# Performance work log

Hardware: AMD Instinct MI355X
Metric: run time of the kernel (lower is better)

The kernel has to match this reference:

```python
import jax, jax.numpy as jnp
import numpy as np

B, L = 4, 2048
D_Q = D_K = D_V = 512
D_MODEL = 512
H = 8  # heads; head dim = D_MODEL // H = 64


def _conv1x1(x, W, b):
    # Conv1d with kernel_size=1 == pointwise linear over channels.
    # x: (B, C_in, L), W: (C_out, C_in), b: (C_out,) -> (B, C_out, L)
    return jnp.einsum('oc,bcl->bol', W, x) + b[None, :, None]


def setup_inputs() -> dict:
    key = jax.random.key(0)
    ks = jax.random.split(key, 12)
    s = 0.02
    return {
        'q': jax.random.normal(ks[0], (B, D_Q, L), jnp.float32),
        'k': jax.random.normal(ks[1], (B, D_K, L), jnp.float32),
        'v': jax.random.normal(ks[2], (B, D_V, L), jnp.float32),
        'input_mask': jnp.ones((B, 1, L), jnp.float32),
        'Wq': jax.random.normal(ks[3], (D_MODEL, D_Q), jnp.float32) * s,
        'bq': jax.random.normal(ks[4], (D_MODEL,), jnp.float32) * s,
        'Wk': jax.random.normal(ks[5], (D_MODEL, D_K), jnp.float32) * s,
        'bk': jax.random.normal(ks[6], (D_MODEL,), jnp.float32) * s,
        'Wv': jax.random.normal(ks[7], (D_MODEL, D_V), jnp.float32) * s,
        'bv': jax.random.normal(ks[8], (D_MODEL,), jnp.float32) * s,
        'Wout': jax.random.normal(ks[9], (D_V, D_MODEL), jnp.float32) * s,
        'bout': jax.random.normal(ks[10], (D_V,), jnp.float32) * s,
    }


def reference(q, k, v, input_mask, Wq, bq, Wk, bk, Wv, bv, Wout, bout):
    Bq, _, Lq = q.shape
    qh = _conv1x1(q, Wq, bq).reshape(Bq, H, -1, Lq)  # (B,H,D,L)
    kh = _conv1x1(k, Wk, bk).reshape(Bq, H, -1, Lq)
    vh = _conv1x1(v, Wv, bv).reshape(Bq, H, -1, Lq)
    Dh = qh.shape[2]
    scale = 1.0 / jnp.sqrt(jnp.asarray(Dh, qh.dtype))
    scores = jnp.einsum('bhdl,bhdn->bhln', qh, kh) * scale  # (B,H,L,L)
    # total_mask = ~input_mask[:, 0:1, :].bool(); True -> masked keys
    pad = input_mask[:, 0:1, :] <= 0.5  # (B,1,L_k)
    scores = jnp.where(pad[:, None, :, :], jnp.asarray(-1e9, scores.dtype), scores)
    attn = jax.nn.softmax(scores, axis=-1)  # attn_dropout is None in module
    out = jnp.einsum('bhdn,bhln->bhdl', vh, attn).reshape(Bq, -1, Lq)  # (B,d_model,L)
    # self.dropout is identity at inference; final 1x1 conv projection
    return _conv1x1(out, Wout, bout)  # (B, d_v, L)
```

## Files before the change

### kernel.cpp

```cpp
#include <hip/hip_runtime.h>
#include <hip/hip_bf16.h>


#define BB  4
#define LL  2048
#define CC  512
#define HH  8
#define DHH 64

typedef __attribute__((ext_vector_type(8)))  short bf16x8;
typedef __attribute__((ext_vector_type(4)))  short bf16x4;
typedef __attribute__((ext_vector_type(16))) float f32x16;
typedef __attribute__((ext_vector_type(2)))  unsigned uint2v;
typedef __attribute__((ext_vector_type(4)))  unsigned uint4v;

using us = unsigned short;

#if __has_builtin(__builtin_amdgcn_exp2f)
#define EXP2(x) __builtin_amdgcn_exp2f(x)
#else
#define EXP2(x) __expf(0.6931471805599453f * (x))
#endif

__device__ __forceinline__ int swz(int r) { return (r + (r >> 3)) & 7; }

__device__ __forceinline__ us f2bu(float x) {
    unsigned u = __float_as_uint(x);
    return (us)((u + 0x7FFFu + ((u >> 16) & 1u)) >> 16);
}
__device__ __forceinline__ unsigned pk2(float a, float b) {
    unsigned r;
    asm("v_cvt_pk_bf16_f32 %0, %1, %2" : "=v"(r) : "v"(a), "v"(b));
    return r;
}
__device__ __forceinline__ bf16x4 pk4(float a, float b, float c, float d) {
    uint2v u; u[0] = pk2(a, b); u[1] = pk2(c, d);
    return __builtin_bit_cast(bf16x4, u);
}

__device__ __forceinline__ void gl16(const void* g, void* l) {
    __builtin_amdgcn_global_load_lds(
        (const __attribute__((address_space(1))) unsigned int*)g,
        (__attribute__((address_space(3))) unsigned int*)l, 16, 0, 0);
}

__device__ __forceinline__ void transpose_body(const float* __restrict__ X,
                                               us* __restrict__ Xt,
                                               int b, int c0, int n0, int t)
{
    __shared__ float T[64][65];

    const float* Xb = X + ((size_t)b * CC + c0) * LL + n0;
    #pragma unroll
    for (int i = 0; i < 4; ++i) {
        const int cl = (t >> 4) + 16 * i, nl = (t & 15) * 4;
        const float4 f = *(const float4*)(Xb + (size_t)cl * LL + nl);
        T[cl][nl + 0] = f.x; T[cl][nl + 1] = f.y;
        T[cl][nl + 2] = f.z; T[cl][nl + 3] = f.w;
    }
    __syncthreads();
    us* Ot = Xt + ((size_t)b * LL + n0) * CC + c0;
    #pragma unroll
    for (int i = 0; i < 2; ++i) {
        const int nl = (t >> 3) + 32 * i, cb = (t & 7) * 8;
        uint4v u;
        #pragma unroll
        for (int j = 0; j < 4; ++j)
            u[j] = pk2(T[cb + 2 * j][nl], T[cb + 2 * j + 1][nl]);
        *(bf16x8*)(Ot + (size_t)nl * CC + cb) = __builtin_bit_cast(bf16x8, u);
    }
}

__global__ __launch_bounds__(256) void transpose_cvt(const float* __restrict__ X,
                                                     us* __restrict__ Xt)
{
    transpose_body(X, Xt, blockIdx.z, blockIdx.y * 64, blockIdx.x * 64, threadIdx.x);
}

__global__ __launch_bounds__(256) void transpose_cvt3(
    const float* __restrict__ Xq, const float* __restrict__ Xk,
    const float* __restrict__ Xv,
    us* __restrict__ X0, us* __restrict__ X1, us* __restrict__ X2)
{
    const int z = blockIdx.z, which = z >> 2, b = z & 3;
    const float* X = which == 0 ? Xq : (which == 1 ? Xk : Xv);
    us* Xt = which == 0 ? X0 : (which == 1 ? X1 : X2);
    transpose_body(X, Xt, b, blockIdx.y * 64, blockIdx.x * 64, threadIdx.x);
}

__global__ __launch_bounds__(256) void cvt_w4(const float* __restrict__ W0,
                                              const float* __restrict__ W1,
                                              const float* __restrict__ W2,
                                              const float* __restrict__ W3,
                                              us* __restrict__ out)
{
    const float* Ws[4] = {W0, W1, W2, W3};
    const float* W = Ws[blockIdx.y];
    us* O = out + (size_t)blockIdx.y * (CC * CC);
    const int i = (blockIdx.x * 256 + threadIdx.x) * 8;
    const float4 f0 = *(const float4*)(W + i);
    const float4 f1 = *(const float4*)(W + i + 4);
    uint4v u;
    u[0] = pk2(f0.x, f0.y); u[1] = pk2(f0.z, f0.w);
    u[2] = pk2(f1.x, f1.y); u[3] = pk2(f1.z, f1.w);
    *(bf16x8*)(O + i) = __builtin_bit_cast(bf16x8, u);
}

__device__ __forceinline__ void proj_body(const us* __restrict__ Xb,
                                          const us* __restrict__ Wm,
                                          const float* __restrict__ bias,
                                          float scale, void* __restrict__ Yv,
                                          int b, int n0, int m0, int t, int mode)
{
    const int lane = t & 63, wave = t >> 6;
    const int quad2 = lane >> 5, l31 = lane & 31;
    const int wr = (wave >> 1) * 64, wc = (wave & 1) * 64;

    __shared__ us As[2][128 * 64];
    __shared__ us Bs[2][128 * 64];
    __shared__ float biasS[128];

    f32x16 acc[2][2];
    #pragma unroll
    for (int mi = 0; mi < 2; ++mi)
        #pragma unroll
        for (int ni = 0; ni < 2; ++ni)
            #pragma unroll
            for (int e = 0; e < 16; ++e) acc[mi][ni][e] = 0.f;

    if (t < 128) biasS[t] = bias[m0 + t];

    #pragma unroll
    for (int i = 0; i < 4; ++i) {
        const int id = i * 256 + t, r = id >> 3, bk = id & 7;
        *(bf16x8*)(As[0] + r * 64 + ((bk ^ swz(r)) * 8)) =
            *(const bf16x8*)(Wm + (size_t)r * CC + bk * 8);
        *(bf16x8*)(Bs[0] + r * 64 + ((bk ^ swz(r)) * 8)) =
            *(const bf16x8*)(Xb + (size_t)(n0 + r) * CC + bk * 8);
    }
    __syncthreads();

    for (int it = 0; it < CC / 64; ++it) {
        const int cur = it & 1, k1 = (it + 1) * 64;

        bf16x8 apre[4], bpre[4];
        if (it + 1 < CC / 64) {
            #pragma unroll
            for (int i = 0; i < 4; ++i) {
                const int id = i * 256 + t, r = id >> 3, bk = id & 7;
                apre[i] = *(const bf16x8*)(Wm + (size_t)r * CC + k1 + bk * 8);
                bpre[i] = *(const bf16x8*)(Xb + (size_t)(n0 + r) * CC + k1 + bk * 8);
            }
        }

        __builtin_amdgcn_s_setprio(1);
        #pragma unroll
        for (int ks = 0; ks < 4; ++ks) {
            const int bk = quad2 + 2 * ks;
            const int ra0 = wr + l31, ra1 = ra0 + 32;
            const int rb0 = wc + l31, rb1 = rb0 + 32;
            const bf16x8 af0 = *(const bf16x8*)(As[cur] + ra0 * 64 + ((bk ^ swz(ra0)) * 8));
            const bf16x8 af1 = *(const bf16x8*)(As[cur] + ra1 * 64 + ((bk ^ swz(ra1)) * 8));
            const bf16x8 bf0 = *(const bf16x8*)(Bs[cur] + rb0 * 64 + ((bk ^ swz(rb0)) * 8));
            const bf16x8 bf1 = *(const bf16x8*)(Bs[cur] + rb1 * 64 + ((bk ^ swz(rb1)) * 8));
            acc[0][0] = __builtin_amdgcn_mfma_f32_32x32x16_bf16(af0, bf0, acc[0][0], 0, 0, 0);
            acc[0][1] = __builtin_amdgcn_mfma_f32_32x32x16_bf16(af0, bf1, acc[0][1], 0, 0, 0);
            acc[1][0] = __builtin_amdgcn_mfma_f32_32x32x16_bf16(af1, bf0, acc[1][0], 0, 0, 0);
            acc[1][1] = __builtin_amdgcn_mfma_f32_32x32x16_bf16(af1, bf1, acc[1][1], 0, 0, 0);
        }
        __builtin_amdgcn_s_setprio(0);

        if (it + 1 < CC / 64) {
            #pragma unroll
            for (int i = 0; i < 4; ++i) {
                const int id = i * 256 + t, r = id >> 3, bk = id & 7;
                *(bf16x8*)(As[1 - cur] + r * 64 + ((bk ^ swz(r)) * 8)) = apre[i];
                *(bf16x8*)(Bs[1 - cur] + r * 64 + ((bk ^ swz(r)) * 8)) = bpre[i];
            }
        }
        __syncthreads();
    }

    #pragma unroll
    for (int mi = 0; mi < 2; ++mi)
        #pragma unroll
        for (int ni = 0; ni < 2; ++ni) {
            const int nloc = wc + ni * 32 + l31;
            if (mode == 0) {
                us* Y = (us*)Yv;
                #pragma unroll
                for (int rg2 = 0; rg2 < 4; ++rg2) {
                    const int rbase = wr + mi * 32 + 8 * rg2 + 4 * quad2;
                    float v0 = (acc[mi][ni][rg2 * 4 + 0] + biasS[rbase + 0]) * scale;
                    float v1 = (acc[mi][ni][rg2 * 4 + 1] + biasS[rbase + 1]) * scale;
                    float v2 = (acc[mi][ni][rg2 * 4 + 2] + biasS[rbase + 2]) * scale;
                    float v3 = (acc[mi][ni][rg2 * 4 + 3] + biasS[rbase + 3]) * scale;
                    const int mg = m0 + rbase;
                    const int h = mg >> 6, d = mg & 63;
                    *(bf16x4*)(Y + (((size_t)(b * HH + h) * LL) + n0 + nloc) * DHH + d) =
                        pk4(v0, v1, v2, v3);
                }
            } else {
                #pragma unroll
                for (int reg = 0; reg < 16; ++reg) {
                    const int row = (reg & 3) + 8 * (reg >> 2) + 4 * quad2;
                    const int mloc = wr + mi * 32 + row;
                    const float v = (acc[mi][ni][reg] + biasS[mloc]) * scale;
                    const size_t addr = ((size_t)b * CC + m0 + mloc) * LL + n0 + nloc;
                    if (mode == 1) ((us*)Yv)[addr] = f2bu(v);
                    else           ((float*)Yv)[addr] = v;
                }
            }
        }
}

template <int MODE>
__global__ __launch_bounds__(256, 2) void proj_gemm(const us* __restrict__ Xt,
                                                    const us* __restrict__ Wb,
                                                    const float* __restrict__ bias,
                                                    float scale,
                                                    void* __restrict__ Yv)
{
    const int b = blockIdx.z, n0 = blockIdx.x * 128, m0 = blockIdx.y * 128;
    proj_body(Xt + (size_t)b * LL * CC, Wb + (size_t)m0 * CC, bias, scale, Yv,
              b, n0, m0, threadIdx.x, MODE);
}

__global__ __launch_bounds__(256, 2) void proj_gemm3(
    const us* __restrict__ X0, const us* __restrict__ X1, const us* __restrict__ X2,
    const us* __restrict__ Wb4,
    const float* __restrict__ bq, const float* __restrict__ bk,
    const float* __restrict__ bv, float scale_q,
    us* __restrict__ qh, us* __restrict__ kh, us* __restrict__ vh)
{
    const int z = blockIdx.z, which = z >> 2, b = z & 3;
    const int n0 = blockIdx.x * 128, m0 = blockIdx.y * 128;
    const us* Xt = which == 0 ? X0 : (which == 1 ? X1 : X2);
    const us* Wb = Wb4 + (size_t)which * (CC * CC);
    const float* bias = which == 0 ? bq : (which == 1 ? bk : bv);
    const float scale = which == 0 ? scale_q : 1.0f;
    us* Yv = which == 0 ? qh : (which == 1 ? kh : vh);
    const int mode = (which == 2) ? 1 : 0;
    proj_body(Xt + (size_t)b * LL * CC, Wb + (size_t)m0 * CC, bias, scale,
              (void*)Yv, b, n0, m0, threadIdx.x, mode);
}

__global__ __launch_bounds__(512, 4) void attn_fwd(
    const us* __restrict__ Qh,
    const us* __restrict__ Kh,
    const us* __restrict__ Vh,
    const float* __restrict__ mask,
    us* __restrict__ ctx)
{
    const int bh = blockIdx.x;
    const int b = bh >> 3, h = bh & 7;
    const int qb = blockIdx.y;
    const int t = threadIdx.x, lane = t & 63, wave = t >> 6;
    const int half = wave >> 2, wv = wave & 3;
    const int quad2 = lane >> 5, l31 = lane & 31;

    __shared__ __align__(16) char SM[81920];

    const float* mb = mask + (size_t)b * LL;
    const int g0 = half * 16;

    const us* Qg = Qh + ((size_t)bh * LL + qb * 128) * DHH;
    #pragma unroll
    for (int i = 0; i < 2; ++i) {
        const int c = t + i * 512, row = c & 127, bk = c >> 7;
        *(bf16x8*)(SM + c * 16) = *(const bf16x8*)(Qg + row * DHH + bk * 8);
    }

    char* KH = SM + 16384 + half * 16384;
    char* VH = SM + 49152 + half * 16384;

    const us* kp = Kh + (size_t)bh * LL * DHH + ((size_t)(g0 * 64) + lane) * DHH + wv * 8;
    const us* vp = Vh + ((size_t)b * CC + h * DHH) * LL + (size_t)lane * LL + g0 * 64 + wv * 8;
    const float* mp = mb + g0 * 64 + lane;

    gl16(kp,      KH + wv * 1024);
    gl16(kp + 32, KH + (wv + 4) * 1024);
    gl16(vp,      VH + wv * 1024);
    gl16(vp + 32, VH + (wv + 4) * 1024);
    kp += 64 * DHH; vp += 64;
    float mval = *mp; mp += 64;
    __syncthreads();

    f32x16 of[2];
    #pragma unroll
    for (int mt = 0; mt < 2; ++mt)
        #pragma unroll
        for (int e = 0; e < 16; ++e) of[mt][e] = 0.f;
    float l_run = 0.f;

    const int rdKV = quad2 * 1024 + l31 * 16;
    const int qrd  = quad2 * 2048 + (wv * 32 + l31) * 16;

    for (int itl = 0; itl < 16; ++itl) {
        const int cur = itl & 1;
        const char* Kc = KH + cur * 8192;
        const char* Vc = VH + cur * 8192;

        float mnext = 0.f;
        if (itl + 1 < 16) {
            char* Kn = KH + (1 - cur) * 8192;
            char* Vn = VH + (1 - cur) * 8192;
            gl16(kp,      Kn + wv * 1024);
            gl16(kp + 32, Kn + (wv + 4) * 1024);
            gl16(vp,      Vn + wv * 1024);
            gl16(vp + 32, Vn + (wv + 4) * 1024);
            kp += 64 * DHH; vp += 64;
            mnext = *mp; mp += 64;
        }

        const unsigned long long mw = __ballot(mval > 0.5f);
        const bool masked = (mw != 0xFFFFFFFFFFFFFFFFull);
        float ps = 0.f;

        #pragma unroll
        for (int mt = 0; mt < 2; ++mt) {
            f32x16 sf;
            #pragma unroll
            for (int e = 0; e < 16; ++e) sf[e] = 0.f;
            __builtin_amdgcn_s_setprio(1);
            #pragma unroll
            for (int ks = 0; ks < 4; ++ks) {
                const bf16x8 qk = *(const bf16x8*)(SM + qrd + ks * 4096);
                const bf16x8 af = *(const bf16x8*)(Kc + rdKV + ks * 2048 + mt * 512);
                sf = __builtin_amdgcn_mfma_f32_32x32x16_bf16(af, qk, sf, 0, 0, 0);
            }
            __builtin_amdgcn_s_setprio(0);

            #pragma unroll
            for (int g = 0; g < 2; ++g) {
                float p[8];
                #pragma unroll
                for (int el = 0; el < 8; ++el) p[el] = EXP2(sf[8 * g + el]);
                if (masked) {
                    #pragma unroll
                    for (int el = 0; el < 8; ++el) {
                        const int row = 32 * mt + 16 * g + (el & 3) + 8 * (el >> 2) + 4 * quad2;
                        p[el] = ((mw >> row) & 1ull) ? p[el] : 0.f;
                    }
                }
                ps += ((p[0] + p[1]) + (p[2] + p[3])) + ((p[4] + p[5]) + (p[6] + p[7]));
                unsigned w0 = pk2(p[0], p[1]);
                unsigned w1 = pk2(p[2], p[3]);
                unsigned w2 = pk2(p[4], p[5]);
                unsigned w3 = pk2(p[6], p[7]);
                asm("v_permlane32_swap_b32 %0, %1" : "+v"(w0), "+v"(w2));
                asm("v_permlane32_swap_b32 %0, %1" : "+v"(w1), "+v"(w3));
                uint4v u; u[0] = w0; u[1] = w1; u[2] = w2; u[3] = w3;
                const bf16x8 pf = __builtin_bit_cast(bf16x8, u);
                const int j = 2 * mt + g;
                __builtin_amdgcn_s_setprio(1);
                of[0] = __builtin_amdgcn_mfma_f32_32x32x16_bf16(
                    *(const bf16x8*)(Vc + rdKV + j * 2048), pf, of[0], 0, 0, 0);
                of[1] = __builtin_amdgcn_mfma_f32_32x32x16_bf16(
                    *(const bf16x8*)(Vc + rdKV + j * 2048 + 512), pf, of[1], 0, 0, 0);
                __builtin_amdgcn_s_setprio(0);
            }
        }
        ps += __shfl_xor(ps, 32, 64);
        l_run += ps;
        mval = mnext;

        __syncthreads();
    }

    float4* OS = (float4*)SM;
    float*  LS = (float*)(SM + 32768);
    const int qg = qb * 128 + wv * 32;
    if (half == 1) {
        #pragma unroll
        for (int mt = 0; mt < 2; ++mt)
            #pragma unroll
            for (int r4 = 0; r4 < 4; ++r4) {
                float4 v;
                v.x = of[mt][r4 * 4 + 0]; v.y = of[mt][r4 * 4 + 1];
                v.z = of[mt][r4 * 4 + 2]; v.w = of[mt][r4 * 4 + 3];
                OS[(wv * 8 + mt * 4 + r4) * 64 + lane] = v;
            }
        LS[wv * 64 + lane] = l_run;
    }
    __syncthreads();
    if (half == 0) {
        l_run += LS[wv * 64 + lane];
        const float inv = 1.0f / l_run;
        us* Cb = ctx + (size_t)b * LL * CC;
        const int q = qg + l31;
        #pragma unroll
        for (int mt = 0; mt < 2; ++mt)
            #pragma unroll
            for (int r4 = 0; r4 < 4; ++r4) {
                const float4 v = OS[(wv * 8 + mt * 4 + r4) * 64 + lane];
                const int d = 32 * mt + 8 * r4 + 4 * quad2;
                *(bf16x4*)(Cb + (size_t)q * CC + h * DHH + d) =
                    pk4((of[mt][r4 * 4 + 0] + v.x) * inv,
                        (of[mt][r4 * 4 + 1] + v.y) * inv,
                        (of[mt][r4 * 4 + 2] + v.z) * inv,
                        (of[mt][r4 * 4 + 3] + v.w) * inv);
            }
    }
}

extern "C" void kernel_launch(void* const* d_in, const int* in_sizes, int n_in,
                              void* d_out, int out_size, void* d_ws, size_t ws_size,
                              hipStream_t stream)
{
    const float* q    = (const float*)d_in[0];
    const float* k    = (const float*)d_in[1];
    const float* v    = (const float*)d_in[2];
    const float* mask = (const float*)d_in[3];
    const float* Wq   = (const float*)d_in[4];
    const float* bq   = (const float*)d_in[5];
    const float* Wk   = (const float*)d_in[6];
    const float* bk   = (const float*)d_in[7];
    const float* Wv   = (const float*)d_in[8];
    const float* bv   = (const float*)d_in[9];
    const float* Wout = (const float*)d_in[10];
    const float* bout = (const float*)d_in[11];

    const size_t TSZ  = (size_t)BB * CC * LL;
    const size_t WSZ  = (size_t)4 * CC * CC;
    const float SCALE_Q = 0.125f * 1.4426950408889634f;

    const dim3 tb(256), gb(256);

    if (ws_size >= (6 * TSZ + WSZ) * sizeof(us)) {
        us* X0  = (us*)d_ws;
        us* X1  = X0 + TSZ;
        us* X2  = X1 + TSZ;
        us* qh  = X2 + TSZ;
        us* kh  = qh + TSZ;
        us* vh  = kh + TSZ;
        us* Wb  = vh + TSZ;
        us* ctx = X0;

        cvt_w4<<<dim3(CC * CC / 2048, 4), tb, 0, stream>>>(Wq, Wk, Wv, Wout, Wb);
        transpose_cvt3<<<dim3(LL / 64, CC / 64, 12), tb, 0, stream>>>(q, k, v, X0, X1, X2);
        proj_gemm3<<<dim3(LL / 128, CC / 128, 12), gb, 0, stream>>>(
            X0, X1, X2, Wb, bq, bk, bv, SCALE_Q, qh, kh, vh);
        attn_fwd<<<dim3(HH * BB, LL / 128), dim3(512), 0, stream>>>(qh, kh, vh, mask, ctx);
        proj_gemm<2><<<dim3(LL / 128, CC / 128, BB), gb, 0, stream>>>(
            ctx, Wb + 3 * (size_t)CC * CC, bout, 1.0f, d_out);
    } else {
        us* Xt  = (us*)d_ws;
        us* qh  = Xt + TSZ;
        us* kh  = qh + TSZ;
        us* vh  = kh + TSZ;
        us* Wb  = vh + TSZ;
        us* ctx = Xt;

        const dim3 tg(LL / 64, CC / 64, BB), gg(LL / 128, CC / 128, BB);

        cvt_w4<<<dim3(CC * CC / 2048, 4), tb, 0, stream>>>(Wq, Wk, Wv, Wout, Wb);
        transpose_cvt<<<tg, tb, 0, stream>>>(q, Xt);
        proj_gemm<0><<<gg, gb, 0, stream>>>(Xt, Wb + 0 * (size_t)CC * CC, bq, SCALE_Q, (void*)qh);
        transpose_cvt<<<tg, tb, 0, stream>>>(k, Xt);
        proj_gemm<0><<<gg, gb, 0, stream>>>(Xt, Wb + 1 * (size_t)CC * CC, bk, 1.0f, (void*)kh);
        transpose_cvt<<<tg, tb, 0, stream>>>(v, Xt);
        proj_gemm<1><<<gg, gb, 0, stream>>>(Xt, Wb + 2 * (size_t)CC * CC, bv, 1.0f, (void*)vh);
        attn_fwd<<<dim3(HH * BB, LL / 128), dim3(512), 0, stream>>>(qh, kh, vh, mask, ctx);
        proj_gemm<2><<<gg, gb, 0, stream>>>(ctx, Wb + 3 * (size_t)CC * CC, bout, 1.0f, d_out);
    }
}
```

Before: 201.9 us.

## Restructure attention to split head dim across waves instead of key range

The attention kernel moves from 512-thread blocks over 128 queries, where two wave halves split the key sequence and then merge partial outputs through shared memory, to 256-thread blocks over 64 queries. Each block now walks all 32 key tiles, and the two wave pairs split the 64 output head-dim columns. Q fragments are held in registers instead of shared memory, and the cross-half reduction and its extra barrier are gone. The cost is that QK^T scores and exponentials are computed twice per query (once per half) and there are twice as many blocks, in exchange for less shared memory per block and no merge epilogue.

```diff
diff --git a/kernel.cpp b/kernel.cpp
--- a/kernel.cpp
+++ b/kernel.cpp
@@ -245,7 +245,7 @@
               (void*)Yv, b, n0, m0, threadIdx.x, mode);
 }
 
-__global__ __launch_bounds__(512, 4) void attn_fwd(
+__global__ __launch_bounds__(256, 3) void attn_fwd(
     const us* __restrict__ Qh,
     const us* __restrict__ Kh,
     const us* __restrict__ Vh,
@@ -256,59 +256,50 @@
     const int b = bh >> 3, h = bh & 7;
     const int qb = blockIdx.y;
     const int t = threadIdx.x, lane = t & 63, wave = t >> 6;
-    const int half = wave >> 2, wv = wave & 3;
+    const int wv = wave & 1, half = wave >> 1;
     const int quad2 = lane >> 5, l31 = lane & 31;
-
-    __shared__ __align__(16) char SM[81920];
-
-    const float* mb = mask + (size_t)b * LL;
-    const int g0 = half * 16;
-
-    const us* Qg = Qh + ((size_t)bh * LL + qb * 128) * DHH;
-    #pragma unroll
-    for (int i = 0; i < 2; ++i) {
-        const int c = t + i * 512, row = c & 127, bk = c >> 7;
-        *(bf16x8*)(SM + c * 16) = *(const bf16x8*)(Qg + row * DHH + bk * 8);
-    }
-
-    char* KH = SM + 16384 + half * 16384;
-    char* VH = SM + 49152 + half * 16384;
-
-    const us* kp = Kh + (size_t)bh * LL * DHH + ((size_t)(g0 * 64) + lane) * DHH + wv * 8;
-    const us* vp = Vh + ((size_t)b * CC + h * DHH) * LL + (size_t)lane * LL + g0 * 64 + wv * 8;
-    const float* mp = mb + g0 * 64 + lane;
-
-    gl16(kp,      KH + wv * 1024);
-    gl16(kp + 32, KH + (wv + 4) * 1024);
-    gl16(vp,      VH + wv * 1024);
-    gl16(vp + 32, VH + (wv + 4) * 1024);
+    const int qg = qb * 64 + wv * 32;
+
+    __shared__ __align__(16) char SM[32768];
+
+    const us* Qbase = Qh + (size_t)bh * LL * DHH;
+    bf16x8 qf[4];
+    #pragma unroll
+    for (int ks = 0; ks < 4; ++ks)
+        qf[ks] = *(const bf16x8*)(Qbase + (size_t)(qg + l31) * DHH + ks * 16 + quad2 * 8);
+
+    const us* kp = Kh + (size_t)bh * LL * DHH + (size_t)lane * DHH + wave * 8;
+    const us* vp = Vh + ((size_t)b * CC + h * DHH) * LL + (size_t)lane * LL + wave * 8;
+    const float* mp = mask + (size_t)b * LL + lane;
+
+    gl16(kp,      SM + wave * 1024);
+    gl16(kp + 32, SM + (wave + 4) * 1024);
+    gl16(vp,      SM + 16384 + wave * 1024);
+    gl16(vp + 32, SM + 16384 + (wave + 4) * 1024);
     kp += 64 * DHH; vp += 64;
     float mval = *mp; mp += 64;
     __syncthreads();
 
-    f32x16 of[2];
-    #pragma unroll
-    for (int mt = 0; mt < 2; ++mt)
-        #pragma unroll
-        for (int e = 0; e < 16; ++e) of[mt][e] = 0.f;
+    f32x16 of;
+    #pragma unroll
+    for (int e = 0; e < 16; ++e) of[e] = 0.f;
     float l_run = 0.f;
 
-    const int rdKV = quad2 * 1024 + l31 * 16;
-    const int qrd  = quad2 * 2048 + (wv * 32 + l31) * 16;
-
-    for (int itl = 0; itl < 16; ++itl) {
+    const int rdF = quad2 * 1024 + l31 * 16;
+
+    for (int itl = 0; itl < 32; ++itl) {
         const int cur = itl & 1;
-        const char* Kc = KH + cur * 8192;
-        const char* Vc = VH + cur * 8192;
+        const char* Kc = SM + cur * 8192;
+        const char* Vc = SM + 16384 + cur * 8192;
 
         float mnext = 0.f;
-        if (itl + 1 < 16) {
-            char* Kn = KH + (1 - cur) * 8192;
-            char* Vn = VH + (1 - cur) * 8192;
-            gl16(kp,      Kn + wv * 1024);
-            gl16(kp + 32, Kn + (wv + 4) * 1024);
-            gl16(vp,      Vn + wv * 1024);
-            gl16(vp + 32, Vn + (wv + 4) * 1024);
+        if (itl + 1 < 32) {
+            char* Kn = SM + (1 - cur) * 8192;
+            char* Vn = SM + 16384 + (1 - cur) * 8192;
+            gl16(kp,      Kn + wave * 1024);
+            gl16(kp + 32, Kn + (wave + 4) * 1024);
+            gl16(vp,      Vn + wave * 1024);
+            gl16(vp + 32, Vn + (wave + 4) * 1024);
             kp += 64 * DHH; vp += 64;
             mnext = *mp; mp += 64;
         }
@@ -325,9 +316,8 @@
             __builtin_amdgcn_s_setprio(1);
             #pragma unroll
             for (int ks = 0; ks < 4; ++ks) {
-                const bf16x8 qk = *(const bf16x8*)(SM + qrd + ks * 4096);
-                const bf16x8 af = *(const bf16x8*)(Kc + rdKV + ks * 2048 + mt * 512);
-                sf = __builtin_amdgcn_mfma_f32_32x32x16_bf16(af, qk, sf, 0, 0, 0);
+                const bf16x8 af = *(const bf16x8*)(Kc + rdF + ks * 2048 + mt * 512);
+                sf = __builtin_amdgcn_mfma_f32_32x32x16_bf16(af, qf[ks], sf, 0, 0, 0);
             }
             __builtin_amdgcn_s_setprio(0);
 
@@ -353,11 +343,9 @@
                 uint4v u; u[0] = w0; u[1] = w1; u[2] = w2; u[3] = w3;
                 const bf16x8 pf = __builtin_bit_cast(bf16x8, u);
                 const int j = 2 * mt + g;
+                const bf16x8 vf = *(const bf16x8*)(Vc + rdF + j * 2048 + half * 512);
                 __builtin_amdgcn_s_setprio(1);
-                of[0] = __builtin_amdgcn_mfma_f32_32x32x16_bf16(
-                    *(const bf16x8*)(Vc + rdKV + j * 2048), pf, of[0], 0, 0, 0);
-                of[1] = __builtin_amdgcn_mfma_f32_32x32x16_bf16(
-                    *(const bf16x8*)(Vc + rdKV + j * 2048 + 512), pf, of[1], 0, 0, 0);
+                of = __builtin_amdgcn_mfma_f32_32x32x16_bf16(vf, pf, of, 0, 0, 0);
                 __builtin_amdgcn_s_setprio(0);
             }
         }
@@ -368,39 +356,15 @@
         __syncthreads();
     }
 
-    float4* OS = (float4*)SM;
-    float*  LS = (float*)(SM + 32768);
-    const int qg = qb * 128 + wv * 32;
-    if (half == 1) {
-        #pragma unroll
-        for (int mt = 0; mt < 2; ++mt)
-            #pragma unroll
-            for (int r4 = 0; r4 < 4; ++r4) {
-                float4 v;
-                v.x = of[mt][r4 * 4 + 0]; v.y = of[mt][r4 * 4 + 1];
-                v.z = of[mt][r4 * 4 + 2]; v.w = of[mt][r4 * 4 + 3];
-                OS[(wv * 8 + mt * 4 + r4) * 64 + lane] = v;
-            }
-        LS[wv * 64 + lane] = l_run;
-    }
-    __syncthreads();
-    if (half == 0) {
-        l_run += LS[wv * 64 + lane];
-        const float inv = 1.0f / l_run;
-        us* Cb = ctx + (size_t)b * LL * CC;
-        const int q = qg + l31;
-        #pragma unroll
-        for (int mt = 0; mt < 2; ++mt)
-            #pragma unroll
-            for (int r4 = 0; r4 < 4; ++r4) {
-                const float4 v = OS[(wv * 8 + mt * 4 + r4) * 64 + lane];
-                const int d = 32 * mt + 8 * r4 + 4 * quad2;
-                *(bf16x4*)(Cb + (size_t)q * CC + h * DHH + d) =
-                    pk4((of[mt][r4 * 4 + 0] + v.x) * inv,
-                        (of[mt][r4 * 4 + 1] + v.y) * inv,
-                        (of[mt][r4 * 4 + 2] + v.z) * inv,
-                        (of[mt][r4 * 4 + 3] + v.w) * inv);
-            }
+    const float inv = 1.0f / l_run;
+    us* Cb = ctx + (size_t)b * LL * CC;
+    const int q = qg + l31;
+    #pragma unroll
+    for (int r4 = 0; r4 < 4; ++r4) {
+        const int d = half * 32 + 8 * r4 + 4 * quad2;
+        *(bf16x4*)(Cb + (size_t)q * CC + h * DHH + d) =
+            pk4(of[r4 * 4 + 0] * inv, of[r4 * 4 + 1] * inv,
+                of[r4 * 4 + 2] * inv, of[r4 * 4 + 3] * inv);
     }
 }
 
@@ -441,7 +405,7 @@
         transpose_cvt3<<<dim3(LL / 64, CC / 64, 12), tb, 0, stream>>>(q, k, v, X0, X1, X2);
         proj_gemm3<<<dim3(LL / 128, CC / 128, 12), gb, 0, stream>>>(
             X0, X1, X2, Wb, bq, bk, bv, SCALE_Q, qh, kh, vh);
-        attn_fwd<<<dim3(HH * BB, LL / 128), dim3(512), 0, stream>>>(qh, kh, vh, mask, ctx);
+        attn_fwd<<<dim3(HH * BB, LL / 64), tb, 0, stream>>>(qh, kh, vh, mask, ctx);
         proj_gemm<2><<<dim3(LL / 128, CC / 128, BB), gb, 0, stream>>>(
             ctx, Wb + 3 * (size_t)CC * CC, bout, 1.0f, d_out);
     } else {
@@ -461,7 +425,7 @@
         proj_gemm<0><<<gg, gb, 0, stream>>>(Xt, Wb + 1 * (size_t)CC * CC, bk, 1.0f, (void*)kh);
         transpose_cvt<<<tg, tb, 0, stream>>>(v, Xt);
         proj_gemm<1><<<gg, gb, 0, stream>>>(Xt, Wb + 2 * (size_t)CC * CC, bv, 1.0f, (void*)vh);
-        attn_fwd<<<dim3(HH * BB, LL / 128), dim3(512), 0, stream>>>(qh, kh, vh, mask, ctx);
+        attn_fwd<<<dim3(HH * BB, LL / 64), tb, 0, stream>>>(qh, kh, vh, mask, ctx);
         proj_gemm<2><<<gg, gb, 0, stream>>>(ctx, Wb + 3 * (size_t)CC * CC, bout, 1.0f, d_out);
     }
 }
```

Measured after the change: 220.6 us. 1.09x slower.
